# Optimization experiments

Hardware: AMD Instinct MI355X
Metric: run time of the kernel (lower is better)

The kernel has to match this reference:

```python
import jax, jax.numpy as jnp
import numpy as np

B, T, C, H, E, K = 2, 2048, 1024, 16, 8, 2
HD = C // H
CAP = int(B * T * K / E * 1.0)  # expert_capacity with capacity_factor=1.0
EPS = 1e-6


def rmsnorm(x):
    return x / jnp.sqrt(jnp.mean(x * x, axis=-1, keepdims=True) + EPS)


def rotary_tables(t_len, hd, base=1024.0):
    steps = hd // 4
    inv = (1.0 / base) ** jnp.linspace(0.0, 1.0, steps)
    inv = jnp.concatenate([inv, jnp.zeros(steps, jnp.float32)])  # [hd//2]
    theta = jnp.arange(t_len, dtype=jnp.float32)[:, None] * inv[None, :]
    return jnp.cos(theta), jnp.sin(theta)


def apply_rot(x, cos, sin):
    d = x.shape[-1] // 2
    x1, x2 = x[..., :d], x[..., d:]
    return jnp.concatenate([x1 * cos + x2 * sin, -x1 * sin + x2 * cos], axis=-1)


def setup_inputs():
    key = jax.random.key(0)
    ks = jax.random.split(key, 9)
    s = 0.02
    return {
        'x': jax.random.normal(ks[0], (B, T, C), jnp.float32),
        'x0': jax.random.normal(ks[1], (B, T, C), jnp.float32),
        'noise': jax.random.normal(ks[2], (B, T, E), jnp.float32),
        'lambdas': jnp.array([1.0, 0.0], jnp.float32),
        'lamb': jnp.array(0.5, jnp.float32),
        'qkv_w': jax.random.normal(ks[3], (3, C, C), jnp.float32) * s,
        'c_proj_w': jax.random.normal(ks[4], (C, C), jnp.float32) * s,
        'c_proj_b': jnp.zeros((C,), jnp.float32),
        'router_w': jax.random.normal(ks[5], (E, C), jnp.float32) * s,
        'router_b': jnp.zeros((E,), jnp.float32),
        'noise_w': jax.random.normal(ks[6], (E, C), jnp.float32) * s,
        'noise_b': jnp.zeros((E,), jnp.float32),
        'ew1': jax.random.normal(ks[7], (E, 4 * C, C), jnp.float32) * s,
        'eb1': jnp.zeros((E, 4 * C), jnp.float32),
        'ew2': jax.random.normal(ks[8], (E, C, 4 * C), jnp.float32) * s,
        'eb2': jnp.zeros((E, C), jnp.float32),
    }


def reference(x, x0, noise, lambdas, lamb, qkv_w, c_proj_w, c_proj_b,
              router_w, router_b, noise_w, noise_b, ew1, eb1, ew2, eb2):
    x = lambdas[0] * x + lambdas[1] * x0
    # ---- causal self-attention (value-residual mix, rms-normed q/k, rotary) ----
    a = rmsnorm(x)
    qkv = jnp.einsum('btc,koc->kbto', a, qkv_w)  # q/k/v = a @ W^T
    heads = lambda t: t.reshape(B, T, H, HD).transpose(0, 2, 1, 3)
    q, k, v = heads(qkv[0]), heads(qkv[1]), heads(qkv[2])
    v = (1.0 - lamb) * v + lamb * v  # v1 defaults to v
    q, k = rmsnorm(q), rmsnorm(k)
    cos, sin = rotary_tables(T, HD)
    cos, sin = cos[None, None], sin[None, None]
    q, k = apply_rot(q, cos, sin), apply_rot(k, cos, sin)
    scores = jnp.einsum('bhqd,bhkd->bhqk', q, k) / jnp.sqrt(jnp.float32(HD))
    causal = jnp.tril(jnp.ones((T, T), bool))
    attn = jax.nn.softmax(jnp.where(causal, scores, -jnp.inf), axis=-1)
    o = jnp.einsum('bhqk,bhkd->bhqd', attn, v).transpose(0, 2, 1, 3).reshape(B, T, C)
    x = x + o @ c_proj_w.T + c_proj_b
    # ---- sparse MoE with noisy top-k router, top-1 dispatch, capacity limit ----
    h = rmsnorm(x)
    logits = h @ router_w.T + router_b
    nlog = h @ noise_w.T + noise_b
    noisy = logits + noise * jax.nn.softplus(nlog)
    topv, topi = jax.lax.top_k(noisy, K)
    gate_k = jax.nn.softmax(topv, axis=-1)  # softmax of sparse(-inf elsewhere) logits
    router = jnp.sum(jax.nn.one_hot(topi, E, dtype=h.dtype) * gate_k[..., None], axis=-2)  # [B,T,E]
    N = B * T
    flat_x = h.reshape(N, C)
    flat_g = router.reshape(N, E)
    eid = jnp.argmax(flat_g, axis=-1)  # dispatch by argmax of gating output (top-1)
    masks = eid[None, :] == jnp.arange(E)[:, None]  # [E,N]
    pos = jnp.where(masks, jnp.arange(N)[None, :], N)
    idx = jnp.sort(pos, axis=1)[:, :CAP]  # first-come-first-served capacity cut
    valid = (idx < N).astype(h.dtype)
    safe = jnp.minimum(idx, N - 1)
    xe = flat_x[safe]  # [E,CAP,C]
    h1 = jnp.square(jax.nn.relu(jnp.einsum('enc,ehc->enh', xe, ew1) + eb1[:, None, :]))
    oe = jnp.einsum('enh,ech->enc', h1, ew2) + eb2[:, None, :]  # dropout=identity (eval)
    g = jnp.take_along_axis(flat_g[safe], jnp.arange(E)[:, None, None], axis=2)[..., 0]  # [E,CAP]
    contrib = oe * (g * valid)[..., None]
    updates = jnp.zeros((N, C), h.dtype).at[safe.reshape(-1)].add(contrib.reshape(-1, C))
    return x + updates.reshape(B, T, C)
```

## Files before the change

kernel.cpp:

```cpp
#include <hip/hip_runtime.h>
#include <math.h>

#define B_    2
#define T_    2048
#define C_    1024
#define H_    16
#define HD_   64
#define E_    8
#define NTOK  4096
#define CAP_  1024
#define FOURC 4096
#define EPS_  1e-6f
#define QBLK  32

typedef __attribute__((ext_vector_type(8))) short bf16x8;
typedef __attribute__((ext_vector_type(4))) float f32x4;

#define OFF_XR   ((size_t)0)
#define OFF_H    ((size_t)4194304)
#define OFF_MISC ((size_t)8388608)
#define OFF_A    (OFF_MISC + 32768)
#define OFF_O    (OFF_A + 4194304)
#define OFF_Q    (OFF_O + 4194304)
#define OFF_K    (OFF_Q + 4194304)
#define OFF_V    (OFF_K + 4194304)

__device__ __forceinline__ float4 ld4(const float* p) { return *(const float4*)p; }

__device__ __forceinline__ unsigned short f2b(float x) {
  unsigned int u = __float_as_uint(x);
  u = (u + 0x7FFFu + ((u >> 16) & 1u)) >> 16;
  return (unsigned short)u;
}

__global__ __launch_bounds__(256)
void k_norm(const float* __restrict__ in, const float* __restrict__ in2,
            const float* __restrict__ lambdas,
            float* __restrict__ rawOut, float* __restrict__ normOut) {
  const int row = blockIdx.x;
  const int t = threadIdx.x;
  const size_t base = (size_t)row * C_ + t * 4;
  float4 v = ld4(in + base);
  float4 m;
  if (in2 != nullptr) {
    const float l0 = lambdas[0], l1 = lambdas[1];
    float4 v2 = ld4(in2 + base);
    m.x = l0 * v.x + l1 * v2.x;
    m.y = l0 * v.y + l1 * v2.y;
    m.z = l0 * v.z + l1 * v2.z;
    m.w = l0 * v.w + l1 * v2.w;
  } else {
    m = v;
  }
  float ss = m.x * m.x + m.y * m.y + m.z * m.z + m.w * m.w;
  #pragma unroll
  for (int off = 32; off > 0; off >>= 1) ss += __shfl_xor(ss, off);
  __shared__ float red[4];
  if ((t & 63) == 0) red[t >> 6] = ss;
  __syncthreads();
  const float tot = red[0] + red[1] + red[2] + red[3];
  const float inv = 1.0f / sqrtf(tot * (1.0f / C_) + EPS_);
  if (rawOut != nullptr) *(float4*)(rawOut + base) = m;
  float4 nm;
  nm.x = m.x * inv; nm.y = m.y * inv; nm.z = m.z * inv; nm.w = m.w * inv;
  *(float4*)(normOut + base) = nm;
}

#define BM 128
#define BN 128
#define BK 16
#define PA 132

template<int MODE>
__global__ __launch_bounds__(256, 2)
void k_gemm(const float* __restrict__ Ag, const float* __restrict__ Bg,
            float* __restrict__ Cg, int Kd, int lda, int ldb,
            const float* __restrict__ bias, const float* __restrict__ resid,
            float* __restrict__ oq, float* __restrict__ ok, float* __restrict__ ov) {
  __shared__ float As[BK * PA];
  __shared__ float Bs[BK * PA];

  const int tid = threadIdx.x;
  const int n0 = blockIdx.x * BN;
  const int m0 = blockIdx.y * BM;

  const int r = tid >> 2;
  const int f4 = (tid & 3) * 4;

  const float* pa0 = Ag + (size_t)(m0 + r) * lda + f4;
  const float* pa1 = Ag + (size_t)(m0 + r + 64) * lda + f4;
  const float* pb0 = Bg + (size_t)(n0 + r) * ldb + f4;
  const float* pb1 = Bg + (size_t)(n0 + r + 64) * ldb + f4;

  float4 ga0, ga1, gb0, gb1;
  const int nkt = Kd >> 4;

  ga0 = ld4(pa0); ga1 = ld4(pa1); gb0 = ld4(pb0); gb1 = ld4(pb1);

  const int tx = tid & 15, ty = tid >> 4;
  float acc[8][8];
  #pragma unroll
  for (int i = 0; i < 8; i++)
    #pragma unroll
    for (int j = 0; j < 8; j++) acc[i][j] = 0.f;

  for (int kt = 0; kt < nkt; kt++) {
    __syncthreads();
    #pragma unroll
    for (int l = 0; l < 4; l++) {
      As[(f4 + l) * PA + r]      = (&ga0.x)[l];
      As[(f4 + l) * PA + r + 64] = (&ga1.x)[l];
      Bs[(f4 + l) * PA + r]      = (&gb0.x)[l];
      Bs[(f4 + l) * PA + r + 64] = (&gb1.x)[l];
    }
    __syncthreads();
    if (kt + 1 < nkt) {
      const int k0 = (kt + 1) * BK;
      ga0 = ld4(pa0 + k0); ga1 = ld4(pa1 + k0);
      gb0 = ld4(pb0 + k0); gb1 = ld4(pb1 + k0);
    }
    #pragma unroll
    for (int kk = 0; kk < BK; kk++) {
      float4 a0 = *(float4*)&As[kk * PA + ty * 4];
      float4 a1 = *(float4*)&As[kk * PA + ty * 4 + 64];
      float4 b0 = *(float4*)&Bs[kk * PA + tx * 4];
      float4 b1 = *(float4*)&Bs[kk * PA + tx * 4 + 64];
      float av[8] = {a0.x, a0.y, a0.z, a0.w, a1.x, a1.y, a1.z, a1.w};
      float bv[8] = {b0.x, b0.y, b0.z, b0.w, b1.x, b1.y, b1.z, b1.w};
      #pragma unroll
      for (int i = 0; i < 8; i++)
        #pragma unroll
        for (int j = 0; j < 8; j++) acc[i][j] += av[i] * bv[j];
    }
  }

  #pragma unroll
  for (int ih = 0; ih < 2; ih++) {
    #pragma unroll
    for (int ii = 0; ii < 4; ii++) {
      const int i = ih * 4 + ii;
      const int m = m0 + ty * 4 + ii + ih * 64;
      #pragma unroll
      for (int jh = 0; jh < 2; jh++) {
        const int n = n0 + tx * 4 + jh * 64;
        float4 vv = make_float4(acc[i][jh * 4 + 0], acc[i][jh * 4 + 1],
                                acc[i][jh * 4 + 2], acc[i][jh * 4 + 3]);
        if (MODE == 0) {
          const int kap = n >> 10;
          const int hh = (n >> 6) & 15;
          const int d = n & 63;
          const int bq = m >> 11, tq = m & 2047;
          float* dst = (kap == 0) ? oq : ((kap == 1) ? ok : ov);
          *(float4*)(dst + ((size_t)((bq * 16 + hh) * 2048 + tq)) * 64 + d) = vv;
        } else {
          float4 bb = ld4(bias + n);
          float4 rr = ld4(resid + (size_t)m * C_ + n);
          vv.x += bb.x + rr.x; vv.y += bb.y + rr.y;
          vv.z += bb.z + rr.z; vv.w += bb.w + rr.w;
          *(float4*)(Cg + (size_t)m * C_ + n) = vv;
        }
      }
    }
  }
}

__global__ __launch_bounds__(256)
void k_qkrot(float* __restrict__ qb, float* __restrict__ kb) {
  const int w = threadIdx.x >> 6, lane = threadIdx.x & 63;
  const int row = blockIdx.x * 4 + w;
  float* buf = (blockIdx.y == 0) ? qb : kb;
  const int t = row & 2047;
  float val = buf[(size_t)row * 64 + lane];
  float ss = val * val;
  #pragma unroll
  for (int off = 32; off > 0; off >>= 1) ss += __shfl_xor(ss, off);
  const float nrm = val / sqrtf(ss * (1.0f / 64.0f) + EPS_);
  const int i = lane & 31;
  float c, s;
  if (i < 16) {
    const float y = (float)i * (1.0f / 15.0f);
    const float inv = exp2f(-10.0f * y);
    const float ang = (float)t * inv;
    c = cosf(ang); s = sinf(ang);
  } else { c = 1.0f; s = 0.0f; }
  const float partner = __shfl_xor(nrm, 32);
  const float out = (lane < 32) ? (nrm * c + partner * s) : (partner * (-s) + nrm * c);
  buf[(size_t)row * 64 + lane] = out;
}

__global__ __launch_bounds__(512, 4)
void k_attn(const float* __restrict__ q, const float* __restrict__ k,
            const float* __restrict__ v, float* __restrict__ o) {
  const int bh = blockIdx.y;
  const int rg = blockIdx.x;
  const int tid = threadIdx.x;
  const int w = tid >> 6, lane = tid & 63;
  __shared__ float qs[QBLK * 64];
  __shared__ float Ks[64 * 64];
  __shared__ float Vt[64 * 64];
  __shared__ float ps[QBLK * 64];
  const size_t base = (size_t)bh * T_ * HD_;

  {
    const int rr = tid >> 4;
    const int d0 = (tid & 15) * 4;
    float4 qv = ld4(q + base + (size_t)(rg * QBLK + rr) * 64 + d0);
    qv.x *= 0.125f; qv.y *= 0.125f; qv.z *= 0.125f; qv.w *= 0.125f;
    *(float4*)&qs[rr * 64 + d0] = qv;
  }

  float oacc[4] = {0.f, 0.f, 0.f, 0.f};
  float lsum[4] = {0.f, 0.f, 0.f, 0.f};
  const int trow0 = rg * QBLK + w * 4;
  const int ktmax = (rg * QBLK + QBLK - 1) >> 6;

  for (int kt = 0; kt <= ktmax; kt++) {
    const int j0 = kt * 64;
    __syncthreads();
    {
      const int d0 = (tid & 15) * 4;
      #pragma unroll
      for (int r2 = 0; r2 < 2; r2++) {
        const int jj = r2 * 32 + (tid >> 4);
        float4 kv = ld4(k + base + (size_t)(j0 + jj) * 64 + d0);
        *(float4*)&Ks[jj * 64 + ((((d0 >> 2) ^ (jj & 7)) << 2))] = kv;
      }
      const int d0v = ((tid >> 4) & 15) * 4;
      #pragma unroll
      for (int r2 = 0; r2 < 2; r2++) {
        const int jj = r2 * 32 + ((tid >> 8) << 4) + (tid & 15);
        float4 vv = ld4(v + base + (size_t)(j0 + jj) * 64 + d0v);
        #pragma unroll
        for (int i = 0; i < 4; i++) {
          const int d = d0v + i;
          Vt[d * 64 + ((((jj >> 2) ^ (d & 7)) << 2) | (jj & 3))] = (&vv.x)[i];
        }
      }
    }
    __syncthreads();

    float s[4] = {0.f, 0.f, 0.f, 0.f};
    #pragma unroll
    for (int d4 = 0; d4 < 16; d4++) {
      float4 k4 = *(float4*)&Ks[lane * 64 + (((d4 ^ (lane & 7)) << 2))];
      #pragma unroll
      for (int rr = 0; rr < 4; rr++) {
        float4 q4 = *(float4*)&qs[(w * 4 + rr) * 64 + d4 * 4];
        s[rr] += k4.x * q4.x + k4.y * q4.y + k4.z * q4.z + k4.w * q4.w;
      }
    }
    #pragma unroll
    for (int rr = 0; rr < 4; rr++) {
      const float p = (j0 + lane <= trow0 + rr) ? expf(s[rr] - 8.0f) : 0.f;
      lsum[rr] += p;
      ps[(w * 4 + rr) * 64 + lane] = p;
    }
    #pragma unroll
    for (int j4 = 0; j4 < 16; j4++) {
      float4 v4 = *(float4*)&Vt[lane * 64 + (((j4 ^ (lane & 7)) << 2))];
      #pragma unroll
      for (int rr = 0; rr < 4; rr++) {
        float4 p4 = *(float4*)&ps[(w * 4 + rr) * 64 + j4 * 4];
        oacc[rr] += p4.x * v4.x + p4.y * v4.y + p4.z * v4.z + p4.w * v4.w;
      }
    }
  }

  const int b = bh >> 4, hh = bh & 15;
  #pragma unroll
  for (int rr = 0; rr < 4; rr++) {
    float tsum = lsum[rr];
    #pragma unroll
    for (int off = 32; off > 0; off >>= 1) tsum += __shfl_xor(tsum, off);
    const int trow = trow0 + rr;
    o[((size_t)(b * 2048 + trow)) * 1024 + hh * 64 + lane] = oacc[rr] / tsum;
  }
}

__global__ __launch_bounds__(256)
void k_router(const float* __restrict__ h, const float* __restrict__ rw,
              const float* __restrict__ rb, const float* __restrict__ nw,
              const float* __restrict__ nb, const float* __restrict__ noise,
              int* __restrict__ eid, float* __restrict__ gate0) {
  const int m = blockIdx.x;
  const int t = threadIdx.x;
  const float4 hv = ld4(h + (size_t)m * C_ + t * 4);
  float pl[E_], pn[E_];
  #pragma unroll
  for (int e2 = 0; e2 < E_; e2++) {
    float4 wv = ld4(rw + (size_t)e2 * C_ + t * 4);
    pl[e2] = hv.x * wv.x + hv.y * wv.y + hv.z * wv.z + hv.w * wv.w;
    float4 nv = ld4(nw + (size_t)e2 * C_ + t * 4);
    pn[e2] = hv.x * nv.x + hv.y * nv.y + hv.z * nv.z + hv.w * nv.w;
  }
  __shared__ float red[16][4];
  const int w = t >> 6, lane = t & 63;
  #pragma unroll
  for (int idx = 0; idx < 16; idx++) {
    float val = (idx < 8) ? pl[idx] : pn[idx - 8];
    #pragma unroll
    for (int off = 32; off > 0; off >>= 1) val += __shfl_xor(val, off);
    if (lane == 0) red[idx][w] = val;
  }
  __syncthreads();
  if (t == 0) {
    float noisy[E_];
    #pragma unroll
    for (int e2 = 0; e2 < E_; e2++) {
      const float lg = red[e2][0] + red[e2][1] + red[e2][2] + red[e2][3] + rb[e2];
      const float nl = red[8 + e2][0] + red[8 + e2][1] + red[8 + e2][2] + red[8 + e2][3] + nb[e2];
      const float sp = fmaxf(nl, 0.f) + log1pf(expf(-fabsf(nl)));
      noisy[e2] = lg + noise[m * E_ + e2] * sp;
    }
    int i0 = 0; float v0 = noisy[0];
    #pragma unroll
    for (int e2 = 1; e2 < E_; e2++)
      if (noisy[e2] > v0) { v0 = noisy[e2]; i0 = e2; }
    float v1 = -INFINITY;
    #pragma unroll
    for (int e2 = 0; e2 < E_; e2++)
      if (e2 != i0 && noisy[e2] > v1) { v1 = noisy[e2]; }
    eid[m] = i0;
    gate0[m] = 1.0f / (1.0f + expf(v1 - v0));
  }
}

__global__ __launch_bounds__(256)
void k_assign(const int* __restrict__ eid, int* __restrict__ slots,
              int* __restrict__ counts) {
  const int t = threadIdx.x;
  int myeid[16];
  #pragma unroll
  for (int i = 0; i < 16; i++) myeid[i] = eid[t * 16 + i];
  int cnt[E_];
  #pragma unroll
  for (int e2 = 0; e2 < E_; e2++) {
    int c = 0;
    #pragma unroll
    for (int i = 0; i < 16; i++) c += (myeid[i] == e2) ? 1 : 0;
    cnt[e2] = c;
  }
  __shared__ int sc[256];
  #pragma unroll
  for (int e2 = 0; e2 < E_; e2++) {
    sc[t] = cnt[e2];
    __syncthreads();
    for (int off = 1; off < 256; off <<= 1) {
      int xv = (t >= off) ? sc[t - off] : 0;
      __syncthreads();
      sc[t] += xv;
      __syncthreads();
    }
    int rank = sc[t] - cnt[e2];
    if (t == 255) counts[e2] = sc[255];
    #pragma unroll
    for (int i = 0; i < 16; i++) {
      if (myeid[i] == e2) {
        if (rank < CAP_) slots[e2 * CAP_ + rank] = t * 16 + i;
        rank++;
      }
    }
    __syncthreads();
  }
}

__global__ __launch_bounds__(256)
void k_cast(const float* __restrict__ in, unsigned short* __restrict__ outp, int n4) {
  for (int i = blockIdx.x * 256 + threadIdx.x; i < n4; i += gridDim.x * 256) {
    float4 vv = ld4(in + (size_t)i * 4);
    ushort4 u;
    u.x = f2b(vv.x); u.y = f2b(vv.y); u.z = f2b(vv.z); u.w = f2b(vv.w);
    *(ushort4*)(outp + (size_t)i * 4) = u;
  }
}

template<int MODE>
__global__ __launch_bounds__(256, 4)
void k_mgemm(const unsigned short* __restrict__ Ab, const unsigned short* __restrict__ Bb,
             int Kd, int lda, int ldb,
             const float* __restrict__ bias,
             unsigned short* __restrict__ h1out, float* __restrict__ fout,
             const int* __restrict__ slots, const int* __restrict__ counts,
             const float* __restrict__ gate, int e0) {
  const int z = blockIdx.z, e = e0 + z;
  int Ne = counts[e]; if (Ne > CAP_) Ne = CAP_;
  const int m0 = blockIdx.y * 128, n0 = blockIdx.x * 128;
  if (m0 >= Ne) return;

  __shared__ __align__(16) unsigned short Asb[128 * 64];
  __shared__ __align__(16) unsigned short Bsb[128 * 64];

  const int tid = threadIdx.x, w = tid >> 6, lane = tid & 63;
  const unsigned short* Az = (MODE == 0) ? Ab : Ab + (size_t)z * CAP_ * FOURC;
  const unsigned short* Bz = Bb + (size_t)z * ((MODE == 0) ? (size_t)FOURC * C_ : (size_t)C_ * FOURC);
  const float* biasz = bias + (size_t)e * ((MODE == 0) ? FOURC : C_);

  const int rsub = lane >> 3;
  const int kc   = lane & 7;
  const int sstore = (kc ^ rsub) * 8;

  int arow[4];
  #pragma unroll
  for (int i = 0; i < 4; i++) {
    const int m = m0 + w * 32 + i * 8 + rsub;
    if (MODE == 0) arow[i] = (m < Ne) ? slots[(size_t)e * CAP_ + m] : 0;
    else           arow[i] = m;
  }

  f32x4 acc[4][4];
  #pragma unroll
  for (int mi = 0; mi < 4; mi++)
    #pragma unroll
    for (int ni = 0; ni < 4; ni++) {
      f32x4 zz = {0.f, 0.f, 0.f, 0.f};
      acc[mi][ni] = zz;
    }

  const int wr = (w >> 1) * 64, wc = (w & 1) * 64;
  const int fr = lane & 15, fq = lane >> 4;
  const int nkt = Kd >> 6;

  for (int kt = 0; kt < nkt; kt++) {
    const int kb = kt * 64;
    bf16x8 ga[4], gb[4];
    #pragma unroll
    for (int i = 0; i < 4; i++) {
      ga[i] = *(const bf16x8*)(Az + (size_t)arow[i] * lda + kb + kc * 8);
      gb[i] = *(const bf16x8*)(Bz + (size_t)(n0 + w * 32 + i * 8 + rsub) * ldb + kb + kc * 8);
    }
    __syncthreads();
    #pragma unroll
    for (int i = 0; i < 4; i++) {
      const int rowL = w * 32 + i * 8 + rsub;
      *(bf16x8*)&Asb[rowL * 64 + sstore] = ga[i];
      *(bf16x8*)&Bsb[rowL * 64 + sstore] = gb[i];
    }
    __syncthreads();
    #pragma unroll
    for (int kk = 0; kk < 2; kk++) {
      const int kcl = kk * 4 + fq;
      bf16x8 af[4], bfr[4];
      #pragma unroll
      for (int t2 = 0; t2 < 4; t2++) {
        const int rowA = wr + t2 * 16 + fr;
        af[t2]  = *(const bf16x8*)&Asb[rowA * 64 + ((kcl ^ (rowA & 7)) << 3)];
        const int rowB = wc + t2 * 16 + fr;
        bfr[t2] = *(const bf16x8*)&Bsb[rowB * 64 + ((kcl ^ (rowB & 7)) << 3)];
      }
      #pragma unroll
      for (int mi = 0; mi < 4; mi++)
        #pragma unroll
        for (int ni = 0; ni < 4; ni++)
          acc[mi][ni] = __builtin_amdgcn_mfma_f32_16x16x32_bf16(af[mi], bfr[ni], acc[mi][ni], 0, 0, 0);
    }
  }

  #pragma unroll
  for (int mi = 0; mi < 4; mi++) {
    #pragma unroll
    for (int reg = 0; reg < 4; reg++) {
      const int m = m0 + wr + mi * 16 + fq * 4 + reg;
      if (MODE == 0) {
        #pragma unroll
        for (int ni = 0; ni < 4; ni++) {
          const int n = n0 + wc + ni * 16 + fr;
          const float r = fmaxf(acc[mi][ni][reg] + biasz[n], 0.f);
          h1out[(size_t)z * CAP_ * FOURC + (size_t)m * FOURC + n] = f2b(r * r);
        }
      } else {
        const int tok = (m < Ne) ? slots[(size_t)e * CAP_ + m] : -1;
        if (tok >= 0) {
          const float gg = gate[tok];
          #pragma unroll
          for (int ni = 0; ni < 4; ni++) {
            const int n = n0 + wc + ni * 16 + fr;
            fout[(size_t)tok * C_ + n] += (acc[mi][ni][reg] + biasz[n]) * gg;
          }
        }
      }
    }
  }
}

extern "C" void kernel_launch(void* const* d_in, const int* in_sizes, int n_in,
                              void* d_out, int out_size, void* d_ws, size_t ws_size,
                              hipStream_t stream) {
  const float* x        = (const float*)d_in[0];
  const float* x0       = (const float*)d_in[1];
  const float* noise    = (const float*)d_in[2];
  const float* lambdas  = (const float*)d_in[3];
  const float* qkv_w    = (const float*)d_in[5];
  const float* c_proj_w = (const float*)d_in[6];
  const float* c_proj_b = (const float*)d_in[7];
  const float* router_w = (const float*)d_in[8];
  const float* router_b = (const float*)d_in[9];
  const float* noise_w  = (const float*)d_in[10];
  const float* noise_b  = (const float*)d_in[11];
  const float* ew1      = (const float*)d_in[12];
  const float* eb1      = (const float*)d_in[13];
  const float* ew2      = (const float*)d_in[14];
  const float* eb2      = (const float*)d_in[15];
  float* out = (float*)d_out;
  float* ws  = (float*)d_ws;

  float* xr  = ws + OFF_XR;
  float* h   = ws + OFF_H;
  int*   eid    = (int*)(ws + OFF_MISC);
  float* gate0  = ws + OFF_MISC + 4096;
  int*   slots  = (int*)(ws + OFF_MISC + 8192);
  int*   counts = (int*)(ws + OFF_MISC + 16384);
  float* a   = ws + OFF_A;
  float* ob  = ws + OFF_O;
  float* qb  = ws + OFF_Q;
  float* kb  = ws + OFF_K;
  float* vb  = ws + OFF_V;

  k_norm<<<NTOK, 256, 0, stream>>>(x, x0, lambdas, xr, a);
  k_gemm<0><<<dim3(24, 32), 256, 0, stream>>>(a, qkv_w, nullptr, 1024, 1024, 1024,
      nullptr, nullptr, qb, kb, vb);
  k_qkrot<<<dim3(16384, 2), 256, 0, stream>>>(qb, kb);
  k_attn<<<dim3(T_ / QBLK, B_ * H_), 512, 0, stream>>>(qb, kb, vb, ob);
  k_gemm<1><<<dim3(8, 32), 256, 0, stream>>>(ob, c_proj_w, out, 1024, 1024, 1024,
      c_proj_b, xr, nullptr, nullptr, nullptr);
  k_norm<<<NTOK, 256, 0, stream>>>(out, nullptr, nullptr, nullptr, h);
  k_router<<<NTOK, 256, 0, stream>>>(h, router_w, router_b, noise_w, noise_b,
                                     noise, eid, gate0);
  k_assign<<<1, 256, 0, stream>>>(eid, slots, counts);

  float* exbase = ws + OFF_A;
  unsigned short* h_b = (unsigned short*)exbase;
  float* chunkbase = exbase + 2097152;
  const size_t ws_floats = ws_size / 4;
  long avail = (long)ws_floats - (long)(OFF_A + 2097152);
  int chunk = (int)(avail / (3L * 2097152));
  if (chunk < 1) chunk = 1;
  if (chunk > E_) chunk = E_;

  k_cast<<<2048, 256, 0, stream>>>(h, h_b, 1048576);

  for (int eb = 0; eb < E_; eb += chunk) {
    const int ce = (E_ - eb < chunk) ? (E_ - eb) : chunk;
    unsigned short* ew1b = (unsigned short*)chunkbase;
    unsigned short* ew2b = (unsigned short*)(chunkbase + (size_t)chunk * 2097152);
    unsigned short* h1b  = (unsigned short*)(chunkbase + (size_t)2 * chunk * 2097152);
    k_cast<<<2048, 256, 0, stream>>>(ew1 + (size_t)eb * 4194304, ew1b, ce * 1048576);
    k_cast<<<2048, 256, 0, stream>>>(ew2 + (size_t)eb * 4194304, ew2b, ce * 1048576);
    k_mgemm<0><<<dim3(32, 8, ce), 256, 0, stream>>>(h_b, ew1b, 1024, 1024, 1024,
        eb1, h1b, nullptr, slots, counts, nullptr, eb);
    k_mgemm<1><<<dim3(8, 8, ce), 256, 0, stream>>>(h1b, ew2b, 4096, 4096, 4096,
        eb2, nullptr, out, slots, counts, gate0, eb);
  }
}
```

Before: 2.004 ms.

## Restructure attention kernel with 4x4 register tiles, prefetch, and heavy-first scheduling

Rewrites the fp32 causal attention kernel to handle 64 query rows per block, with 256 threads each computing a 4x4 register tile of scores and outputs. This replaces the old one-key-per-lane dot products and should cut LDS traffic per FMA. The next K/V tile is prefetched into registers while the current one is computed, and blocks are ordered so the longest causal row groups launch first. It also switches to __expf and vectorized output stores. In exchange, register pressure is higher and there are fewer, larger blocks.

```diff
diff --git a/kernel.cpp b/kernel.cpp
--- a/kernel.cpp
+++ b/kernel.cpp
@@ -11,7 +11,6 @@
 #define CAP_  1024
 #define FOURC 4096
 #define EPS_  1e-6f
-#define QBLK  32
 
 typedef __attribute__((ext_vector_type(8))) short bf16x8;
 typedef __attribute__((ext_vector_type(4))) float f32x4;
@@ -188,92 +187,155 @@
   buf[(size_t)row * 64 + lane] = out;
 }
 
-__global__ __launch_bounds__(512, 4)
+__global__ __launch_bounds__(256, 2)
 void k_attn(const float* __restrict__ q, const float* __restrict__ k,
             const float* __restrict__ v, float* __restrict__ o) {
-  const int bh = blockIdx.y;
-  const int rg = blockIdx.x;
+  const int gid = blockIdx.x;
+  const int rg = 31 - (gid >> 5);
+  const int bh = gid & 31;
   const int tid = threadIdx.x;
   const int w = tid >> 6, lane = tid & 63;
-  __shared__ float qs[QBLK * 64];
+  const int rq = lane >> 4;
+  const int cq = lane & 15;
+  __shared__ float qs[64 * 64];
   __shared__ float Ks[64 * 64];
   __shared__ float Vt[64 * 64];
-  __shared__ float ps[QBLK * 64];
-  const size_t base = (size_t)bh * T_ * HD_;
+  __shared__ float ps[64 * 64];
+  const size_t base = (size_t)bh * (T_ * HD_);
+  const int row0 = rg * 64;
 
   {
-    const int rr = tid >> 4;
-    const int d0 = (tid & 15) * 4;
-    float4 qv = ld4(q + base + (size_t)(rg * QBLK + rr) * 64 + d0);
-    qv.x *= 0.125f; qv.y *= 0.125f; qv.z *= 0.125f; qv.w *= 0.125f;
-    *(float4*)&qs[rr * 64 + d0] = qv;
-  }
-
-  float oacc[4] = {0.f, 0.f, 0.f, 0.f};
-  float lsum[4] = {0.f, 0.f, 0.f, 0.f};
-  const int trow0 = rg * QBLK + w * 4;
-  const int ktmax = (rg * QBLK + QBLK - 1) >> 6;
-
-  for (int kt = 0; kt <= ktmax; kt++) {
+    const int c = tid & 15;
+    #pragma unroll
+    for (int p = 0; p < 4; p++) {
+      const int r = p * 16 + (tid >> 4);
+      float4 qv = ld4(q + base + (size_t)(row0 + r) * 64 + c * 4);
+      qv.x *= 0.125f; qv.y *= 0.125f; qv.z *= 0.125f; qv.w *= 0.125f;
+      *(float4*)&qs[r * 64 + ((c ^ ((r >> 2) & 7)) << 2)] = qv;
+    }
+  }
+
+  float oacc[4][4];
+  float lsum[4];
+  #pragma unroll
+  for (int i = 0; i < 4; i++) {
+    lsum[i] = 0.f;
+    #pragma unroll
+    for (int j = 0; j < 4; j++) oacc[i][j] = 0.f;
+  }
+
+  const int swzR = ((w * 4 + rq) & 7);
+  const int swzC = (cq & 7);
+  const int rbase = w * 16 + rq * 4;
+
+  float4 kpf[4], vpf[4];
+  {
+    const int c = tid & 15;
+    #pragma unroll
+    for (int p = 0; p < 4; p++) {
+      const int r = p * 16 + (tid >> 4);
+      kpf[p] = ld4(k + base + (size_t)r * 64 + c * 4);
+      vpf[p] = ld4(v + base + (size_t)r * 64 + c * 4);
+    }
+  }
+
+  for (int kt = 0; kt <= rg; kt++) {
     const int j0 = kt * 64;
     __syncthreads();
     {
-      const int d0 = (tid & 15) * 4;
-      #pragma unroll
-      for (int r2 = 0; r2 < 2; r2++) {
-        const int jj = r2 * 32 + (tid >> 4);
-        float4 kv = ld4(k + base + (size_t)(j0 + jj) * 64 + d0);
-        *(float4*)&Ks[jj * 64 + ((((d0 >> 2) ^ (jj & 7)) << 2))] = kv;
-      }
-      const int d0v = ((tid >> 4) & 15) * 4;
-      #pragma unroll
-      for (int r2 = 0; r2 < 2; r2++) {
-        const int jj = r2 * 32 + ((tid >> 8) << 4) + (tid & 15);
-        float4 vv = ld4(v + base + (size_t)(j0 + jj) * 64 + d0v);
+      const int c = tid & 15;
+      #pragma unroll
+      for (int p = 0; p < 4; p++) {
+        const int r = p * 16 + (tid >> 4);
+        *(float4*)&Ks[r * 64 + ((c ^ ((r >> 2) & 7)) << 2)] = kpf[p];
         #pragma unroll
         for (int i = 0; i < 4; i++) {
-          const int d = d0v + i;
-          Vt[d * 64 + ((((jj >> 2) ^ (d & 7)) << 2) | (jj & 3))] = (&vv.x)[i];
+          const int d = c * 4 + i;
+          Vt[d * 64 + ((((r >> 2) ^ ((d >> 2) & 7)) << 2) | (r & 3))] = (&vpf[p].x)[i];
         }
       }
     }
     __syncthreads();
-
-    float s[4] = {0.f, 0.f, 0.f, 0.f};
+    if (kt < rg) {
+      const int c = tid & 15;
+      #pragma unroll
+      for (int p = 0; p < 4; p++) {
+        const int r = p * 16 + (tid >> 4);
+        kpf[p] = ld4(k + base + (size_t)(j0 + 64 + r) * 64 + c * 4);
+        vpf[p] = ld4(v + base + (size_t)(j0 + 64 + r) * 64 + c * 4);
+      }
+    }
+
+    float acc[4][4];
+    #pragma unroll
+    for (int i = 0; i < 4; i++)
+      #pragma unroll
+      for (int j = 0; j < 4; j++) acc[i][j] = 0.f;
+
     #pragma unroll
     for (int d4 = 0; d4 < 16; d4++) {
-      float4 k4 = *(float4*)&Ks[lane * 64 + (((d4 ^ (lane & 7)) << 2))];
-      #pragma unroll
-      for (int rr = 0; rr < 4; rr++) {
-        float4 q4 = *(float4*)&qs[(w * 4 + rr) * 64 + d4 * 4];
-        s[rr] += k4.x * q4.x + k4.y * q4.y + k4.z * q4.z + k4.w * q4.w;
-      }
-    }
-    #pragma unroll
-    for (int rr = 0; rr < 4; rr++) {
-      const float p = (j0 + lane <= trow0 + rr) ? expf(s[rr] - 8.0f) : 0.f;
-      lsum[rr] += p;
-      ps[(w * 4 + rr) * 64 + lane] = p;
-    }
-    #pragma unroll
-    for (int j4 = 0; j4 < 16; j4++) {
-      float4 v4 = *(float4*)&Vt[lane * 64 + (((j4 ^ (lane & 7)) << 2))];
-      #pragma unroll
-      for (int rr = 0; rr < 4; rr++) {
-        float4 p4 = *(float4*)&ps[(w * 4 + rr) * 64 + j4 * 4];
-        oacc[rr] += p4.x * v4.x + p4.y * v4.y + p4.z * v4.z + p4.w * v4.w;
-      }
-    }
+      float4 kk[4], qq[4];
+      #pragma unroll
+      for (int i = 0; i < 4; i++) {
+        kk[i] = *(float4*)&Ks[(cq * 4 + i) * 64 + ((d4 ^ swzC) << 2)];
+        qq[i] = *(float4*)&qs[(rbase + i) * 64 + ((d4 ^ swzR) << 2)];
+      }
+      #pragma unroll
+      for (int ri = 0; ri < 4; ri++)
+        #pragma unroll
+        for (int ji = 0; ji < 4; ji++) {
+          acc[ri][ji] += qq[ri].x * kk[ji].x + qq[ri].y * kk[ji].y
+                       + qq[ri].z * kk[ji].z + qq[ri].w * kk[ji].w;
+        }
+    }
+
+    #pragma unroll
+    for (int ri = 0; ri < 4; ri++) {
+      const int r = row0 + rbase + ri;
+      float4 pv;
+      #pragma unroll
+      for (int ji = 0; ji < 4; ji++) {
+        const float p = (j0 + cq * 4 + ji <= r) ? __expf(acc[ri][ji] - 8.0f) : 0.f;
+        (&pv.x)[ji] = p;
+        lsum[ri] += p;
+      }
+      *(float4*)&ps[(rbase + ri) * 64 + ((cq ^ swzR) << 2)] = pv;
+    }
+
+    #pragma unroll
+    for (int jc = 0; jc < 16; jc++) {
+      float4 pp[4], vv[4];
+      #pragma unroll
+      for (int i = 0; i < 4; i++) {
+        pp[i] = *(float4*)&ps[(rbase + i) * 64 + ((jc ^ swzR) << 2)];
+        vv[i] = *(float4*)&Vt[(cq * 4 + i) * 64 + ((jc ^ swzC) << 2)];
+      }
+      #pragma unroll
+      for (int ri = 0; ri < 4; ri++)
+        #pragma unroll
+        for (int di = 0; di < 4; di++) {
+          oacc[ri][di] += pp[ri].x * vv[di].x + pp[ri].y * vv[di].y
+                        + pp[ri].z * vv[di].z + pp[ri].w * vv[di].w;
+        }
+    }
+  }
+
+  #pragma unroll
+  for (int ri = 0; ri < 4; ri++) {
+    float t2 = lsum[ri];
+    #pragma unroll
+    for (int off = 1; off < 16; off <<= 1) t2 += __shfl_xor(t2, off);
+    lsum[ri] = t2;
   }
 
   const int b = bh >> 4, hh = bh & 15;
   #pragma unroll
-  for (int rr = 0; rr < 4; rr++) {
-    float tsum = lsum[rr];
-    #pragma unroll
-    for (int off = 32; off > 0; off >>= 1) tsum += __shfl_xor(tsum, off);
-    const int trow = trow0 + rr;
-    o[((size_t)(b * 2048 + trow)) * 1024 + hh * 64 + lane] = oacc[rr] / tsum;
+  for (int ri = 0; ri < 4; ri++) {
+    const int r = row0 + rbase + ri;
+    const float inv = 1.0f / lsum[ri];
+    float4 ov = make_float4(oacc[ri][0] * inv, oacc[ri][1] * inv,
+                            oacc[ri][2] * inv, oacc[ri][3] * inv);
+    *(float4*)(o + ((size_t)(b * 2048 + r)) * 1024 + hh * 64 + cq * 4) = ov;
   }
 }
 
@@ -519,7 +581,7 @@
   k_gemm<0><<<dim3(24, 32), 256, 0, stream>>>(a, qkv_w, nullptr, 1024, 1024, 1024,
       nullptr, nullptr, qb, kb, vb);
   k_qkrot<<<dim3(16384, 2), 256, 0, stream>>>(qb, kb);
-  k_attn<<<dim3(T_ / QBLK, B_ * H_), 512, 0, stream>>>(qb, kb, vb, ob);
+  k_attn<<<1024, 256, 0, stream>>>(qb, kb, vb, ob);
   k_gemm<1><<<dim3(8, 32), 256, 0, stream>>>(ob, c_proj_w, out, 1024, 1024, 1024,
       c_proj_b, xr, nullptr, nullptr, nullptr);
   k_norm<<<NTOK, 256, 0, stream>>>(out, nullptr, nullptr, nullptr, h);
```

Result: slower. 5.340 ms (+166.4%).
